# Optimization experiments

Hardware: AMD Instinct MI355X
Metric: run time of the kernel (lower is better)

Reference implementation:

```python
import jax, jax.numpy as jnp
import numpy as np

MODEL_DIM = 768
N_HEAD = 12
HEAD_DIM = MODEL_DIM // N_HEAD
B, S = 2, 2048


def setup_inputs() -> dict:
    key = jax.random.key(0)
    ks = jax.random.split(key, 11)
    sc = 1.0 / np.sqrt(MODEL_DIM)
    inp = {
        "q": jax.random.normal(ks[0], (B, S, MODEL_DIM), jnp.float32),
        "k": jax.random.normal(ks[1], (B, S, MODEL_DIM), jnp.float32),
        "v": jax.random.normal(ks[2], (B, S, MODEL_DIM), jnp.float32),
        "wq_w": jax.random.normal(ks[3], (MODEL_DIM, MODEL_DIM), jnp.float32) * sc,
        "wq_b": jax.random.normal(ks[4], (MODEL_DIM,), jnp.float32) * sc,
        "wk_w": jax.random.normal(ks[5], (MODEL_DIM, MODEL_DIM), jnp.float32) * sc,
        "wk_b": jax.random.normal(ks[6], (MODEL_DIM,), jnp.float32) * sc,
        "wv_w": jax.random.normal(ks[7], (MODEL_DIM, MODEL_DIM), jnp.float32) * sc,
        "wv_b": jax.random.normal(ks[8], (MODEL_DIM,), jnp.float32) * sc,
        "wo_w": jax.random.normal(ks[9], (MODEL_DIM, MODEL_DIM), jnp.float32) * sc,
        "wo_b": jax.random.normal(ks[10], (MODEL_DIM,), jnp.float32) * sc,
    }
    return inp


def _split_heads(x):
    b, s, _ = x.shape
    return x.reshape(b, s, N_HEAD, HEAD_DIM).transpose(0, 2, 1, 3)  # [B,H,S,Dh]


def reference(q, k, v, wq_w, wq_b, wk_w, wk_b, wv_w, wv_b, wo_w, wo_b):
    # Linear projections (torch Linear: x @ W.T + b)
    query = _split_heads(q @ wq_w.T + wq_b)
    key = _split_heads(k @ wk_w.T + wk_b)
    value = _split_heads(v @ wv_w.T + wv_b)
    scale = 1.0 / np.sqrt(HEAD_DIM)
    scores = jnp.einsum("bhqd,bhkd->bhqk", query, key) * scale
    attn_weights = jax.nn.softmax(scores, axis=-1)
    context = jnp.einsum("bhqk,bhkd->bhqd", attn_weights, value)
    b, h, s, dh = context.shape
    context = context.transpose(0, 2, 1, 3).reshape(b, s, MODEL_DIM)
    output = context @ wo_w.T + wo_b
    return output, attn_weights
```

## Files before the change

kernel.cpp:

```cpp
#include <hip/hip_runtime.h>
#include <stdint.h>

#define S_LEN   2048
#define NH      12
#define NBH     24
#define DMODEL  768
#define OUT0    3145728
#define SD      131072
#define WSZ     589824

#define QB_OFF   0
#define KB_OFF   3145728
#define VB_OFF   6291456
#define WQ_OFF   9437184
#define WK_OFF   10027008
#define WV_OFF   10616832
#define WO_OFF   11206656
#define QH_OFF   11796480
#define KH_OFF   14942208
#define VT_OFF   18087936
#define CTX_OFF  21233664

typedef __attribute__((ext_vector_type(4))) float          f32x4;
typedef __attribute__((ext_vector_type(8))) __bf16         bf16x8;
typedef __attribute__((ext_vector_type(4))) float          fl4;
typedef __attribute__((ext_vector_type(4))) unsigned short us4;

__device__ __forceinline__ unsigned short f2bf(float f) {
  union { float f; unsigned u; } x; x.f = f;
  return (unsigned short)((x.u + 0x7FFFu + ((x.u >> 16) & 1u)) >> 16);
}

__device__ __forceinline__ float fexp2(float x) {
#if __has_builtin(__builtin_amdgcn_exp2f)
  return __builtin_amdgcn_exp2f(x);
#else
  return exp2f(x);
#endif
}

__device__ __forceinline__ void gld16(const void* g, void* l) {
  __builtin_amdgcn_global_load_lds((__attribute__((address_space(1))) void*)g,
                                   (__attribute__((address_space(3))) void*)l,
                                   16, 0, 0);
}

#define MFMA(a, b, c) __builtin_amdgcn_mfma_f32_16x16x32_bf16((a), (b), (c), 0, 0, 0)

__global__ __launch_bounds__(256) void cvt_kernel(
    const float* __restrict__ q, const float* __restrict__ k, const float* __restrict__ v,
    const float* __restrict__ wq, const float* __restrict__ wk, const float* __restrict__ wv,
    const float* __restrict__ wo, unsigned short* __restrict__ ws)
{
  const int seg = blockIdx.y;
  const float* src; unsigned short* dst; int n; float sc = 1.0f;
  if      (seg == 0) { src = q;  dst = ws + QB_OFF; n = OUT0; }
  else if (seg == 1) { src = k;  dst = ws + KB_OFF; n = OUT0; }
  else if (seg == 2) { src = v;  dst = ws + VB_OFF; n = OUT0; }
  else if (seg == 3) { src = wq; dst = ws + WQ_OFF; n = WSZ; sc = 0.125f; }
  else if (seg == 4) { src = wk; dst = ws + WK_OFF; n = WSZ; }
  else if (seg == 5) { src = wv; dst = ws + WV_OFF; n = WSZ; }
  else               { src = wo; dst = ws + WO_OFF; n = WSZ; }
  const int i4 = blockIdx.x * blockDim.x + threadIdx.x;
  if (i4 * 4 >= n) return;
  fl4 f = ((const fl4*)src)[i4];
  us4 o;
  o.x = f2bf(f.x * sc); o.y = f2bf(f.y * sc);
  o.z = f2bf(f.z * sc); o.w = f2bf(f.w * sc);
  ((us4*)dst)[i4] = o;
}

__global__ __launch_bounds__(256, 2) void proj_qkv(
    unsigned short* __restrict__ ws, const float* __restrict__ bq,
    const float* __restrict__ bk, const float* __restrict__ bv)
{
  __shared__ __align__(16) unsigned short As[128 * 64];
  __shared__ __align__(16) unsigned short Bs[128 * 64];
  const int mat = blockIdx.z;
  const unsigned short* X = ws + (size_t)mat * OUT0;
  const unsigned short* W = ws + WQ_OFF + (size_t)mat * WSZ;
  const float* bias = (mat == 0) ? bq : ((mat == 1) ? bk : bv);
  const float bsc = (mat == 0) ? 0.125f : 1.0f;
  unsigned short* dst = ws + QH_OFF + (size_t)mat * OUT0;
  const int m0 = blockIdx.y * 128, n0 = blockIdx.x * 128;
  const int tid = threadIdx.x, lane = tid & 63, w = tid >> 6;
  const int wm = w >> 1, wn = w & 1, qd = lane >> 4, ln = lane & 15;
  const int srow = lane >> 3, scol = (lane & 7) * 8;

  f32x4 acc[4][4] = {};
  for (int k0 = 0; k0 < 768; k0 += 64) {
#pragma unroll
    for (int i = 0; i < 4; i++) {
      const int row = (w * 4 + i) * 8 + srow;
      gld16(X + (size_t)(m0 + row) * 768 + k0 + scol, As + (w * 4 + i) * 512);
      gld16(W + (size_t)(n0 + row) * 768 + k0 + scol, Bs + (w * 4 + i) * 512);
    }
    __syncthreads();
    bf16x8 a[4][2], b[4][2];
#pragma unroll
    for (int kst = 0; kst < 2; kst++) {
#pragma unroll
      for (int mt = 0; mt < 4; mt++)
        a[mt][kst] = *(const bf16x8*)(As + (wm * 64 + mt * 16 + ln) * 64 + kst * 32 + qd * 8);
#pragma unroll
      for (int nt = 0; nt < 4; nt++)
        b[nt][kst] = *(const bf16x8*)(Bs + (wn * 64 + nt * 16 + ln) * 64 + kst * 32 + qd * 8);
    }
#pragma unroll
    for (int mt = 0; mt < 4; mt++)
#pragma unroll
      for (int nt = 0; nt < 4; nt++) {
        acc[mt][nt] = MFMA(a[mt][0], b[nt][0], acc[mt][nt]);
        acc[mt][nt] = MFMA(a[mt][1], b[nt][1], acc[mt][nt]);
      }
    __syncthreads();
  }
#pragma unroll
  for (int nt = 0; nt < 4; nt++) {
    const int n = n0 + wn * 64 + nt * 16 + ln;
    const float bvv = bias[n] * bsc;
    const int h = n >> 6, d = n & 63;
    if (mat < 2) {
#pragma unroll
      for (int mt = 0; mt < 4; mt++)
#pragma unroll
        for (int r = 0; r < 4; r++) {
          const int m = m0 + wm * 64 + mt * 16 + qd * 4 + r;
          const int bb = m >> 11, s = m & 2047;
          dst[(size_t)(bb * NH + h) * SD + (size_t)s * 64 + d] = f2bf(acc[mt][nt][r] + bvv);
        }
    } else {
#pragma unroll
      for (int mt = 0; mt < 4; mt++) {
        const int m = m0 + wm * 64 + mt * 16 + qd * 4;
        const int bb = m >> 11, s = m & 2047;
        us4 o;
        o.x = f2bf(acc[mt][nt][0] + bvv); o.y = f2bf(acc[mt][nt][1] + bvv);
        o.z = f2bf(acc[mt][nt][2] + bvv); o.w = f2bf(acc[mt][nt][3] + bvv);
        *(us4*)(dst + (size_t)(bb * NH + h) * SD + (size_t)d * S_LEN + s) = o;
      }
    }
  }
}

__global__ __launch_bounds__(256, 2) void attn_kernel(
    unsigned short* __restrict__ ws, float* __restrict__ attn_out)
{
  __shared__ __align__(16) unsigned short Qs[128 * 64];
  __shared__ __align__(16) unsigned short KP[128 * 136];
  __shared__ __align__(16) unsigned short Vts[64 * 128];
  __shared__ float rsum[128];

  const int bh = blockIdx.y;
  const int i0 = blockIdx.x * 128;
  const unsigned short* Qg = ws + QH_OFF + (size_t)bh * SD + (size_t)i0 * 64;
  const unsigned short* Kg = ws + KH_OFF + (size_t)bh * SD;
  const unsigned short* Vg = ws + VT_OFF + (size_t)bh * SD;
  float* attnB = attn_out + (size_t)bh * S_LEN * S_LEN + (size_t)i0 * S_LEN;
  unsigned short* ctxB = ws + CTX_OFF + ((size_t)(bh / NH) * S_LEN + i0) * DMODEL + (bh % NH) * 64;

  const int tid = threadIdx.x, lane = tid & 63, w = tid >> 6;
  const int wm = w >> 1, wn = w & 1, qd = lane >> 4, ln = lane & 15;
  const float LOG2E = 1.4426950408889634f;

#pragma unroll
  for (int i = 0; i < 4; i++) gld16(Qg + (w * 4 + i) * 512 + lane * 8, Qs + (w * 4 + i) * 512);
  if (tid < 128) rsum[tid] = 0.f;
  __syncthreads();

  bf16x8 aq[4][2];
#pragma unroll
  for (int kst = 0; kst < 2; kst++)
#pragma unroll
    for (int mt = 0; mt < 4; mt++)
      aq[mt][kst] = *(const bf16x8*)(Qs + (wm * 64 + mt * 16 + ln) * 64 + kst * 32 + qd * 8);

  float psum[4][4] = {};
  for (int jt = 0; jt < 16; jt++) {
    const unsigned short* Kt = Kg + jt * 8192;
#pragma unroll
    for (int i = 0; i < 4; i++) gld16(Kt + (w * 4 + i) * 512 + lane * 8, KP + (w * 4 + i) * 512);
    __syncthreads();
    bf16x8 b[4][2];
#pragma unroll
    for (int kst = 0; kst < 2; kst++)
#pragma unroll
      for (int nt = 0; nt < 4; nt++)
        b[nt][kst] = *(const bf16x8*)(KP + (wn * 64 + nt * 16 + ln) * 64 + kst * 32 + qd * 8);
#pragma unroll
    for (int mt = 0; mt < 4; mt++)
#pragma unroll
      for (int nt = 0; nt < 4; nt++) {
        f32x4 c = {0.f, 0.f, 0.f, 0.f};
        c = MFMA(aq[mt][0], b[nt][0], c);
        c = MFMA(aq[mt][1], b[nt][1], c);
#pragma unroll
        for (int r = 0; r < 4; r++) psum[mt][r] += fexp2(c[r] * LOG2E);
      }
    __syncthreads();
  }
#pragma unroll
  for (int mt = 0; mt < 4; mt++)
#pragma unroll
    for (int r = 0; r < 4; r++) {
      float vv = psum[mt][r];
      vv += __shfl_xor(vv, 1); vv += __shfl_xor(vv, 2);
      vv += __shfl_xor(vv, 4); vv += __shfl_xor(vv, 8);
      if (ln == 0) atomicAdd(&rsum[wm * 64 + mt * 16 + qd * 4 + r], vv);
    }
  __syncthreads();
  if (tid < 128) rsum[tid] = 1.0f / rsum[tid];
  __syncthreads();
  float rv[4][4];
#pragma unroll
  for (int mt = 0; mt < 4; mt++)
#pragma unroll
    for (int r = 0; r < 4; r++) rv[mt][r] = rsum[wm * 64 + mt * 16 + qd * 4 + r];

  f32x4 ctx[4][2] = {};
  for (int jt = 0; jt < 16; jt++) {
    const unsigned short* Kt = Kg + jt * 8192;
#pragma unroll
    for (int i = 0; i < 4; i++) {
      gld16(Kt + (w * 4 + i) * 512 + lane * 8, KP + (w * 4 + i) * 512);
      const int d = (w * 4 + i) * 4 + qd;
      gld16(Vg + (size_t)d * S_LEN + jt * 128 + ln * 8, Vts + (w * 4 + i) * 512);
    }
    __syncthreads();
    bf16x8 b[4][2];
#pragma unroll
    for (int kst = 0; kst < 2; kst++)
#pragma unroll
      for (int nt = 0; nt < 4; nt++)
        b[nt][kst] = *(const bf16x8*)(KP + (wn * 64 + nt * 16 + ln) * 64 + kst * 32 + qd * 8);
    float pv[4][4][4];
#pragma unroll
    for (int mt = 0; mt < 4; mt++)
#pragma unroll
      for (int nt = 0; nt < 4; nt++) {
        f32x4 c = {0.f, 0.f, 0.f, 0.f};
        c = MFMA(aq[mt][0], b[nt][0], c);
        c = MFMA(aq[mt][1], b[nt][1], c);
#pragma unroll
        for (int r = 0; r < 4; r++)
          pv[mt][nt][r] = fexp2(c[r] * LOG2E) * rv[mt][r];
      }
#pragma unroll
    for (int mt = 0; mt < 4; mt++)
#pragma unroll
      for (int r = 0; r < 4; r++) {
        float* drow = attnB + (size_t)(wm * 64 + mt * 16 + qd * 4 + r) * S_LEN + jt * 128 + wn * 64 + ln;
#pragma unroll
        for (int nt = 0; nt < 4; nt++) drow[nt * 16] = pv[mt][nt][r];
      }
    __syncthreads();
#pragma unroll
    for (int mt = 0; mt < 4; mt++)
#pragma unroll
      for (int nt = 0; nt < 4; nt++)
#pragma unroll
        for (int r = 0; r < 4; r++)
          KP[(wm * 64 + mt * 16 + qd * 4 + r) * 136 + wn * 64 + nt * 16 + ln] = f2bf(pv[mt][nt][r]);
    __syncthreads();
#pragma unroll
    for (int kst = 0; kst < 4; kst++) {
      bf16x8 pa[4], vb[2];
#pragma unroll
      for (int mt = 0; mt < 4; mt++)
        pa[mt] = *(const bf16x8*)(KP + (wm * 64 + mt * 16 + ln) * 136 + kst * 32 + qd * 8);
#pragma unroll
      for (int nt = 0; nt < 2; nt++)
        vb[nt] = *(const bf16x8*)(Vts + (wn * 32 + nt * 16 + ln) * 128 + kst * 32 + qd * 8);
#pragma unroll
      for (int mt = 0; mt < 4; mt++)
#pragma unroll
        for (int nt = 0; nt < 2; nt++)
          ctx[mt][nt] = MFMA(pa[mt], vb[nt], ctx[mt][nt]);
    }
    __syncthreads();
  }
#pragma unroll
  for (int mt = 0; mt < 4; mt++)
#pragma unroll
    for (int nt = 0; nt < 2; nt++)
#pragma unroll
      for (int r = 0; r < 4; r++) {
        const int row = wm * 64 + mt * 16 + qd * 4 + r;
        ctxB[(size_t)row * DMODEL + wn * 32 + nt * 16 + ln] = f2bf(ctx[mt][nt][r]);
      }
}

__global__ __launch_bounds__(256, 2) void out_proj(
    const unsigned short* __restrict__ ws, const float* __restrict__ wob,
    float* __restrict__ out)
{
  __shared__ __align__(16) unsigned short As[128 * 64];
  __shared__ __align__(16) unsigned short Bs[128 * 64];
  const unsigned short* X = ws + CTX_OFF;
  const unsigned short* W = ws + WO_OFF;
  const int m0 = blockIdx.y * 128, n0 = blockIdx.x * 128;
  const int tid = threadIdx.x, lane = tid & 63, w = tid >> 6;
  const int wm = w >> 1, wn = w & 1, qd = lane >> 4, ln = lane & 15;
  const int srow = lane >> 3, scol = (lane & 7) * 8;

  f32x4 acc[4][4] = {};
  for (int k0 = 0; k0 < 768; k0 += 64) {
#pragma unroll
    for (int i = 0; i < 4; i++) {
      const int row = (w * 4 + i) * 8 + srow;
      gld16(X + (size_t)(m0 + row) * 768 + k0 + scol, As + (w * 4 + i) * 512);
      gld16(W + (size_t)(n0 + row) * 768 + k0 + scol, Bs + (w * 4 + i) * 512);
    }
    __syncthreads();
    bf16x8 a[4][2], b[4][2];
#pragma unroll
    for (int kst = 0; kst < 2; kst++) {
#pragma unroll
      for (int mt = 0; mt < 4; mt++)
        a[mt][kst] = *(const bf16x8*)(As + (wm * 64 + mt * 16 + ln) * 64 + kst * 32 + qd * 8);
#pragma unroll
      for (int nt = 0; nt < 4; nt++)
        b[nt][kst] = *(const bf16x8*)(Bs + (wn * 64 + nt * 16 + ln) * 64 + kst * 32 + qd * 8);
    }
#pragma unroll
    for (int mt = 0; mt < 4; mt++)
#pragma unroll
      for (int nt = 0; nt < 4; nt++) {
        acc[mt][nt] = MFMA(a[mt][0], b[nt][0], acc[mt][nt]);
        acc[mt][nt] = MFMA(a[mt][1], b[nt][1], acc[mt][nt]);
      }
    __syncthreads();
  }
#pragma unroll
  for (int nt = 0; nt < 4; nt++) {
    const int n = n0 + wn * 64 + nt * 16 + ln;
    const float bvv = wob[n];
#pragma unroll
    for (int mt = 0; mt < 4; mt++)
#pragma unroll
      for (int r = 0; r < 4; r++) {
        const int m = m0 + wm * 64 + mt * 16 + qd * 4 + r;
        out[(size_t)m * DMODEL + n] = acc[mt][nt][r] + bvv;
      }
  }
}

extern "C" void kernel_launch(void* const* d_in, const int* in_sizes, int n_in,
                              void* d_out, int out_size, void* d_ws, size_t ws_size,
                              hipStream_t stream)
{
  const float* q  = (const float*)d_in[0];
  const float* k  = (const float*)d_in[1];
  const float* v  = (const float*)d_in[2];
  const float* wq = (const float*)d_in[3];
  const float* bq = (const float*)d_in[4];
  const float* wk = (const float*)d_in[5];
  const float* bk = (const float*)d_in[6];
  const float* wv = (const float*)d_in[7];
  const float* bv = (const float*)d_in[8];
  const float* wo = (const float*)d_in[9];
  const float* bo = (const float*)d_in[10];
  unsigned short* ws = (unsigned short*)d_ws;
  float* out = (float*)d_out;

  cvt_kernel<<<dim3(3072, 7), 256, 0, stream>>>(q, k, v, wq, wk, wv, wo, ws);
  proj_qkv<<<dim3(6, 32, 3), 256, 0, stream>>>(ws, bq, bk, bv);
  attn_kernel<<<dim3(16, 24), 256, 0, stream>>>(ws, out + OUT0);
  out_proj<<<dim3(6, 32), 256, 0, stream>>>(ws, bo, out);
}
```

Baseline: 574.6 us.

## Double-buffer LDS tiles with XOR swizzle and vectorized attn stores in all GEMMs

Adds LDS double buffering with manual vmcnt waits and raw barriers to the projection GEMMs and both attention passes, so the next K/weight tile loads while MFMAs run on the current one. LDS layouts are XOR-swizzled to avoid bank conflicts. The attention kernel swaps the MFMA operand order so each lane holds four consecutive keys, which lets it write attn weights as 16-byte vector stores and reduce row sums with fewer shuffles. It also stages P in a separate swizzled buffer, at the cost of relying on hand-tuned waitcnt values that must match the outstanding load counts.

```diff
diff --git a/kernel.cpp b/kernel.cpp
--- a/kernel.cpp
+++ b/kernel.cpp
@@ -23,6 +23,7 @@
 
 typedef __attribute__((ext_vector_type(4))) float          f32x4;
 typedef __attribute__((ext_vector_type(8))) __bf16         bf16x8;
+typedef __attribute__((ext_vector_type(4))) __bf16         bf16x4;
 typedef __attribute__((ext_vector_type(4))) float          fl4;
 typedef __attribute__((ext_vector_type(4))) unsigned short us4;
 
@@ -46,6 +47,8 @@
 }
 
 #define MFMA(a, b, c) __builtin_amdgcn_mfma_f32_16x16x32_bf16((a), (b), (c), 0, 0, 0)
+#define MEMBAR() asm volatile("" ::: "memory")
+#define SBAR()   __builtin_amdgcn_s_barrier()
 
 __global__ __launch_bounds__(256) void cvt_kernel(
     const float* __restrict__ q, const float* __restrict__ k, const float* __restrict__ v,
@@ -74,8 +77,8 @@
     unsigned short* __restrict__ ws, const float* __restrict__ bq,
     const float* __restrict__ bk, const float* __restrict__ bv)
 {
-  __shared__ __align__(16) unsigned short As[128 * 64];
-  __shared__ __align__(16) unsigned short Bs[128 * 64];
+  __shared__ __align__(16) unsigned short As[2][8192];
+  __shared__ __align__(16) unsigned short Bs[2][8192];
   const int mat = blockIdx.z;
   const unsigned short* X = ws + (size_t)mat * OUT0;
   const unsigned short* W = ws + WQ_OFF + (size_t)mat * WSZ;
@@ -85,26 +88,38 @@
   const int m0 = blockIdx.y * 128, n0 = blockIdx.x * 128;
   const int tid = threadIdx.x, lane = tid & 63, w = tid >> 6;
   const int wm = w >> 1, wn = w & 1, qd = lane >> 4, ln = lane & 15;
-  const int srow = lane >> 3, scol = (lane & 7) * 8;
+  const int srow = lane >> 3, sc8 = ((lane & 7) ^ srow) * 8;
+
+#pragma unroll
+  for (int i = 0; i < 4; i++) {
+    const int row = (w * 4 + i) * 8 + srow;
+    gld16(X + (size_t)(m0 + row) * 768 + sc8, &As[0][(w * 4 + i) * 512]);
+    gld16(W + (size_t)(n0 + row) * 768 + sc8, &Bs[0][(w * 4 + i) * 512]);
+  }
 
   f32x4 acc[4][4] = {};
-  for (int k0 = 0; k0 < 768; k0 += 64) {
+  for (int kk = 0; kk < 12; kk++) {
+    const int knx = (kk == 11) ? 0 : (kk + 1);
+    const int nb = (kk + 1) & 1;
 #pragma unroll
     for (int i = 0; i < 4; i++) {
       const int row = (w * 4 + i) * 8 + srow;
-      gld16(X + (size_t)(m0 + row) * 768 + k0 + scol, As + (w * 4 + i) * 512);
-      gld16(W + (size_t)(n0 + row) * 768 + k0 + scol, Bs + (w * 4 + i) * 512);
-    }
-    __syncthreads();
+      gld16(X + (size_t)(m0 + row) * 768 + knx * 64 + sc8, &As[nb][(w * 4 + i) * 512]);
+      gld16(W + (size_t)(n0 + row) * 768 + knx * 64 + sc8, &Bs[nb][(w * 4 + i) * 512]);
+    }
+    asm volatile("s_waitcnt vmcnt(8)" ::: "memory");
+    SBAR();
+    const unsigned short* Ac = As[kk & 1];
+    const unsigned short* Bc = Bs[kk & 1];
     bf16x8 a[4][2], b[4][2];
 #pragma unroll
     for (int kst = 0; kst < 2; kst++) {
 #pragma unroll
       for (int mt = 0; mt < 4; mt++)
-        a[mt][kst] = *(const bf16x8*)(As + (wm * 64 + mt * 16 + ln) * 64 + kst * 32 + qd * 8);
+        a[mt][kst] = *(const bf16x8*)(Ac + (wm * 64 + mt * 16 + ln) * 64 + (((kst * 4 + qd) ^ (ln & 7)) * 8));
 #pragma unroll
       for (int nt = 0; nt < 4; nt++)
-        b[nt][kst] = *(const bf16x8*)(Bs + (wn * 64 + nt * 16 + ln) * 64 + kst * 32 + qd * 8);
+        b[nt][kst] = *(const bf16x8*)(Bc + (wn * 64 + nt * 16 + ln) * 64 + (((kst * 4 + qd) ^ (ln & 7)) * 8));
     }
 #pragma unroll
     for (int mt = 0; mt < 4; mt++)
@@ -113,7 +128,8 @@
         acc[mt][nt] = MFMA(a[mt][0], b[nt][0], acc[mt][nt]);
         acc[mt][nt] = MFMA(a[mt][1], b[nt][1], acc[mt][nt]);
       }
-    __syncthreads();
+    MEMBAR();
+    SBAR();
   }
 #pragma unroll
   for (int nt = 0; nt < 4; nt++) {
@@ -141,15 +157,19 @@
       }
     }
   }
+  asm volatile("s_waitcnt vmcnt(0)" ::: "memory");
 }
 
 __global__ __launch_bounds__(256, 2) void attn_kernel(
     unsigned short* __restrict__ ws, float* __restrict__ attn_out)
 {
-  __shared__ __align__(16) unsigned short Qs[128 * 64];
-  __shared__ __align__(16) unsigned short KP[128 * 136];
-  __shared__ __align__(16) unsigned short Vts[64 * 128];
-  __shared__ float rsum[128];
+  __shared__ __align__(16) unsigned short lds[40960];
+  unsigned short* K0 = lds;
+  unsigned short* K1 = lds + 8192;
+  unsigned short* Vt = lds + 16384;
+  unsigned short* P  = lds + 24576;
+  float* rsum        = (float*)(lds + 24576);
+  unsigned short* Qs = lds + 32768;
 
   const int bh = blockIdx.y;
   const int i0 = blockIdx.x * 128;
@@ -161,123 +181,149 @@
 
   const int tid = threadIdx.x, lane = tid & 63, w = tid >> 6;
   const int wm = w >> 1, wn = w & 1, qd = lane >> 4, ln = lane & 15;
+  const int srow = lane >> 3, sc8 = ((lane & 7) ^ srow) * 8;
   const float LOG2E = 1.4426950408889634f;
 
 #pragma unroll
-  for (int i = 0; i < 4; i++) gld16(Qg + (w * 4 + i) * 512 + lane * 8, Qs + (w * 4 + i) * 512);
+  for (int i = 0; i < 4; i++) {
+    const int row = (w * 4 + i) * 8 + srow;
+    gld16(Qg + (size_t)row * 64 + sc8, Qs + (w * 4 + i) * 512);
+  }
+  MEMBAR();
+#pragma unroll
+  for (int i = 0; i < 4; i++) {
+    const int row = (w * 4 + i) * 8 + srow;
+    gld16(Kg + (size_t)row * 64 + sc8, K0 + (w * 4 + i) * 512);
+  }
   if (tid < 128) rsum[tid] = 0.f;
-  __syncthreads();
-
-  bf16x8 aq[4][2];
+  asm volatile("s_waitcnt vmcnt(4) lgkmcnt(0)" ::: "memory");
+  SBAR();
+
+  bf16x8 bq[4][2];
 #pragma unroll
   for (int kst = 0; kst < 2; kst++)
 #pragma unroll
-    for (int mt = 0; mt < 4; mt++)
-      aq[mt][kst] = *(const bf16x8*)(Qs + (wm * 64 + mt * 16 + ln) * 64 + kst * 32 + qd * 8);
-
-  float psum[4][4] = {};
+    for (int qt = 0; qt < 4; qt++)
+      bq[qt][kst] = *(const bf16x8*)(Qs + (wm * 64 + qt * 16 + ln) * 64 + (((kst * 4 + qd) ^ (ln & 7)) * 8));
+
+  float psl[4] = {0.f, 0.f, 0.f, 0.f};
   for (int jt = 0; jt < 16; jt++) {
-    const unsigned short* Kt = Kg + jt * 8192;
-#pragma unroll
-    for (int i = 0; i < 4; i++) gld16(Kt + (w * 4 + i) * 512 + lane * 8, KP + (w * 4 + i) * 512);
-    __syncthreads();
-    bf16x8 b[4][2];
+    const unsigned short* Kn = Kg + (size_t)((jt + 1) & 15) * 8192;
+    unsigned short* Kw = (jt & 1) ? K0 : K1;
+#pragma unroll
+    for (int i = 0; i < 4; i++) {
+      const int row = (w * 4 + i) * 8 + srow;
+      gld16(Kn + (size_t)row * 64 + sc8, Kw + (w * 4 + i) * 512);
+    }
+    asm volatile("s_waitcnt vmcnt(4)" ::: "memory");
+    SBAR();
+    const unsigned short* Kc = (jt & 1) ? K1 : K0;
+    bf16x8 ak[4][2];
 #pragma unroll
     for (int kst = 0; kst < 2; kst++)
 #pragma unroll
-      for (int nt = 0; nt < 4; nt++)
-        b[nt][kst] = *(const bf16x8*)(KP + (wn * 64 + nt * 16 + ln) * 64 + kst * 32 + qd * 8);
-#pragma unroll
-    for (int mt = 0; mt < 4; mt++)
-#pragma unroll
-      for (int nt = 0; nt < 4; nt++) {
+      for (int kt = 0; kt < 4; kt++)
+        ak[kt][kst] = *(const bf16x8*)(Kc + (wn * 64 + kt * 16 + ln) * 64 + (((kst * 4 + qd) ^ (ln & 7)) * 8));
+#pragma unroll
+    for (int qt = 0; qt < 4; qt++)
+#pragma unroll
+      for (int kt = 0; kt < 4; kt++) {
         f32x4 c = {0.f, 0.f, 0.f, 0.f};
-        c = MFMA(aq[mt][0], b[nt][0], c);
-        c = MFMA(aq[mt][1], b[nt][1], c);
-#pragma unroll
-        for (int r = 0; r < 4; r++) psum[mt][r] += fexp2(c[r] * LOG2E);
-      }
-    __syncthreads();
-  }
-#pragma unroll
-  for (int mt = 0; mt < 4; mt++)
-#pragma unroll
-    for (int r = 0; r < 4; r++) {
-      float vv = psum[mt][r];
-      vv += __shfl_xor(vv, 1); vv += __shfl_xor(vv, 2);
-      vv += __shfl_xor(vv, 4); vv += __shfl_xor(vv, 8);
-      if (ln == 0) atomicAdd(&rsum[wm * 64 + mt * 16 + qd * 4 + r], vv);
-    }
-  __syncthreads();
-  if (tid < 128) rsum[tid] = 1.0f / rsum[tid];
-  __syncthreads();
-  float rv[4][4];
-#pragma unroll
-  for (int mt = 0; mt < 4; mt++)
-#pragma unroll
-    for (int r = 0; r < 4; r++) rv[mt][r] = rsum[wm * 64 + mt * 16 + qd * 4 + r];
+        c = MFMA(ak[kt][0], bq[qt][0], c);
+        c = MFMA(ak[kt][1], bq[qt][1], c);
+        psl[qt] += fexp2(c[0] * LOG2E) + fexp2(c[1] * LOG2E)
+                 + fexp2(c[2] * LOG2E) + fexp2(c[3] * LOG2E);
+      }
+    MEMBAR();
+    SBAR();
+  }
+#pragma unroll
+  for (int qt = 0; qt < 4; qt++) {
+    float v = psl[qt];
+    v += __shfl_xor(v, 16);
+    v += __shfl_xor(v, 32);
+    psl[qt] = v;
+  }
+  if (lane < 16) {
+#pragma unroll
+    for (int qt = 0; qt < 4; qt++)
+      atomicAdd(&rsum[wm * 64 + qt * 16 + lane], psl[qt]);
+  }
+  asm volatile("s_waitcnt lgkmcnt(0)" ::: "memory");
+  SBAR();
+  float rv[4];
+#pragma unroll
+  for (int qt = 0; qt < 4; qt++) rv[qt] = 1.0f / rsum[wm * 64 + qt * 16 + ln];
 
   f32x4 ctx[4][2] = {};
   for (int jt = 0; jt < 16; jt++) {
-    const unsigned short* Kt = Kg + jt * 8192;
 #pragma unroll
     for (int i = 0; i < 4; i++) {
-      gld16(Kt + (w * 4 + i) * 512 + lane * 8, KP + (w * 4 + i) * 512);
       const int d = (w * 4 + i) * 4 + qd;
-      gld16(Vg + (size_t)d * S_LEN + jt * 128 + ln * 8, Vts + (w * 4 + i) * 512);
-    }
-    __syncthreads();
-    bf16x8 b[4][2];
+      const int csw = ((lane & 15) ^ ((i & 1) * 4 + qd)) * 8;
+      gld16(Vg + (size_t)d * S_LEN + jt * 128 + csw, Vt + (w * 4 + i) * 512);
+    }
+    MEMBAR();
+    const unsigned short* Kn = Kg + (size_t)((jt + 1) & 15) * 8192;
+    unsigned short* Kw = (jt & 1) ? K0 : K1;
+#pragma unroll
+    for (int i = 0; i < 4; i++) {
+      const int row = (w * 4 + i) * 8 + srow;
+      gld16(Kn + (size_t)row * 64 + sc8, Kw + (w * 4 + i) * 512);
+    }
+    asm volatile("s_waitcnt vmcnt(8)" ::: "memory");
+    SBAR();
+
+    const unsigned short* Kc = (jt & 1) ? K1 : K0;
+    bf16x8 ak[4][2];
 #pragma unroll
     for (int kst = 0; kst < 2; kst++)
 #pragma unroll
-      for (int nt = 0; nt < 4; nt++)
-        b[nt][kst] = *(const bf16x8*)(KP + (wn * 64 + nt * 16 + ln) * 64 + kst * 32 + qd * 8);
-    float pv[4][4][4];
-#pragma unroll
-    for (int mt = 0; mt < 4; mt++)
-#pragma unroll
-      for (int nt = 0; nt < 4; nt++) {
+      for (int kt = 0; kt < 4; kt++)
+        ak[kt][kst] = *(const bf16x8*)(Kc + (wn * 64 + kt * 16 + ln) * 64 + (((kst * 4 + qd) ^ (ln & 7)) * 8));
+
+#pragma unroll
+    for (int qt = 0; qt < 4; qt++) {
+      const int qrow = wm * 64 + qt * 16 + ln;
+      float* aRow = attnB + (size_t)qrow * S_LEN + jt * 128 + wn * 64 + qd * 4;
+      unsigned short* pRow = P + qrow * 128;
+      const int r7x8 = (ln & 7) * 8;
+#pragma unroll
+      for (int kt = 0; kt < 4; kt++) {
         f32x4 c = {0.f, 0.f, 0.f, 0.f};
-        c = MFMA(aq[mt][0], b[nt][0], c);
-        c = MFMA(aq[mt][1], b[nt][1], c);
-#pragma unroll
-        for (int r = 0; r < 4; r++)
-          pv[mt][nt][r] = fexp2(c[r] * LOG2E) * rv[mt][r];
-      }
-#pragma unroll
-    for (int mt = 0; mt < 4; mt++)
-#pragma unroll
-      for (int r = 0; r < 4; r++) {
-        float* drow = attnB + (size_t)(wm * 64 + mt * 16 + qd * 4 + r) * S_LEN + jt * 128 + wn * 64 + ln;
-#pragma unroll
-        for (int nt = 0; nt < 4; nt++) drow[nt * 16] = pv[mt][nt][r];
-      }
-    __syncthreads();
-#pragma unroll
-    for (int mt = 0; mt < 4; mt++)
-#pragma unroll
-      for (int nt = 0; nt < 4; nt++)
-#pragma unroll
-        for (int r = 0; r < 4; r++)
-          KP[(wm * 64 + mt * 16 + qd * 4 + r) * 136 + wn * 64 + nt * 16 + ln] = f2bf(pv[mt][nt][r]);
-    __syncthreads();
+        c = MFMA(ak[kt][0], bq[qt][0], c);
+        c = MFMA(ak[kt][1], bq[qt][1], c);
+        f32x4 pv;
+        pv.x = fexp2(c[0] * LOG2E) * rv[qt];
+        pv.y = fexp2(c[1] * LOG2E) * rv[qt];
+        pv.z = fexp2(c[2] * LOG2E) * rv[qt];
+        pv.w = fexp2(c[3] * LOG2E) * rv[qt];
+        *(f32x4*)(aRow + kt * 16) = pv;
+        bf16x4 pb;
+        pb.x = (__bf16)pv.x; pb.y = (__bf16)pv.y;
+        pb.z = (__bf16)pv.z; pb.w = (__bf16)pv.w;
+        *(bf16x4*)(pRow + ((wn * 64 + kt * 16 + qd * 4) ^ r7x8)) = pb;
+      }
+    }
+    asm volatile("s_waitcnt vmcnt(20) lgkmcnt(0)" ::: "memory");
+    SBAR();
 #pragma unroll
     for (int kst = 0; kst < 4; kst++) {
       bf16x8 pa[4], vb[2];
 #pragma unroll
       for (int mt = 0; mt < 4; mt++)
-        pa[mt] = *(const bf16x8*)(KP + (wm * 64 + mt * 16 + ln) * 136 + kst * 32 + qd * 8);
+        pa[mt] = *(const bf16x8*)(P + (wm * 64 + mt * 16 + ln) * 128 + ((kst * 32 + qd * 8) ^ ((ln & 7) * 8)));
 #pragma unroll
       for (int nt = 0; nt < 2; nt++)
-        vb[nt] = *(const bf16x8*)(Vts + (wn * 32 + nt * 16 + ln) * 128 + kst * 32 + qd * 8);
+        vb[nt] = *(const bf16x8*)(Vt + (wn * 32 + nt * 16 + ln) * 128 + (((kst * 4 + qd) ^ (ln & 7)) * 8));
 #pragma unroll
       for (int mt = 0; mt < 4; mt++)
 #pragma unroll
         for (int nt = 0; nt < 2; nt++)
           ctx[mt][nt] = MFMA(pa[mt], vb[nt], ctx[mt][nt]);
     }
-    __syncthreads();
+    MEMBAR();
+    SBAR();
   }
 #pragma unroll
   for (int mt = 0; mt < 4; mt++)
@@ -288,39 +334,52 @@
         const int row = wm * 64 + mt * 16 + qd * 4 + r;
         ctxB[(size_t)row * DMODEL + wn * 32 + nt * 16 + ln] = f2bf(ctx[mt][nt][r]);
       }
+  asm volatile("s_waitcnt vmcnt(0)" ::: "memory");
 }
 
 __global__ __launch_bounds__(256, 2) void out_proj(
     const unsigned short* __restrict__ ws, const float* __restrict__ wob,
     float* __restrict__ out)
 {
-  __shared__ __align__(16) unsigned short As[128 * 64];
-  __shared__ __align__(16) unsigned short Bs[128 * 64];
+  __shared__ __align__(16) unsigned short As[2][8192];
+  __shared__ __align__(16) unsigned short Bs[2][8192];
   const unsigned short* X = ws + CTX_OFF;
   const unsigned short* W = ws + WO_OFF;
   const int m0 = blockIdx.y * 128, n0 = blockIdx.x * 128;
   const int tid = threadIdx.x, lane = tid & 63, w = tid >> 6;
   const int wm = w >> 1, wn = w & 1, qd = lane >> 4, ln = lane & 15;
-  const int srow = lane >> 3, scol = (lane & 7) * 8;
+  const int srow = lane >> 3, sc8 = ((lane & 7) ^ srow) * 8;
+
+#pragma unroll
+  for (int i = 0; i < 4; i++) {
+    const int row = (w * 4 + i) * 8 + srow;
+    gld16(X + (size_t)(m0 + row) * 768 + sc8, &As[0][(w * 4 + i) * 512]);
+    gld16(W + (size_t)(n0 + row) * 768 + sc8, &Bs[0][(w * 4 + i) * 512]);
+  }
 
   f32x4 acc[4][4] = {};
-  for (int k0 = 0; k0 < 768; k0 += 64) {
+  for (int kk = 0; kk < 12; kk++) {
+    const int knx = (kk == 11) ? 0 : (kk + 1);
+    const int nb = (kk + 1) & 1;
 #pragma unroll
     for (int i = 0; i < 4; i++) {
       const int row = (w * 4 + i) * 8 + srow;
-      gld16(X + (size_t)(m0 + row) * 768 + k0 + scol, As + (w * 4 + i) * 512);
-      gld16(W + (size_t)(n0 + row) * 768 + k0 + scol, Bs + (w * 4 + i) * 512);
-    }
-    __syncthreads();
+      gld16(X + (size_t)(m0 + row) * 768 + knx * 64 + sc8, &As[nb][(w * 4 + i) * 512]);
+      gld16(W + (size_t)(n0 + row) * 768 + knx * 64 + sc8, &Bs[nb][(w * 4 + i) * 512]);
+    }
+    asm volatile("s_waitcnt vmcnt(8)" ::: "memory");
+    SBAR();
+    const unsigned short* Ac = As[kk & 1];
+    const unsigned short* Bc = Bs[kk & 1];
     bf16x8 a[4][2], b[4][2];
 #pragma unroll
     for (int kst = 0; kst < 2; kst++) {
 #pragma unroll
       for (int mt = 0; mt < 4; mt++)
-        a[mt][kst] = *(const bf16x8*)(As + (wm * 64 + mt * 16 + ln) * 64 + kst * 32 + qd * 8);
+        a[mt][kst] = *(const bf16x8*)(Ac + (wm * 64 + mt * 16 + ln) * 64 + (((kst * 4 + qd) ^ (ln & 7)) * 8));
 #pragma unroll
       for (int nt = 0; nt < 4; nt++)
-        b[nt][kst] = *(const bf16x8*)(Bs + (wn * 64 + nt * 16 + ln) * 64 + kst * 32 + qd * 8);
+        b[nt][kst] = *(const bf16x8*)(Bc + (wn * 64 + nt * 16 + ln) * 64 + (((kst * 4 + qd) ^ (ln & 7)) * 8));
     }
 #pragma unroll
     for (int mt = 0; mt < 4; mt++)
@@ -329,7 +388,8 @@
         acc[mt][nt] = MFMA(a[mt][0], b[nt][0], acc[mt][nt]);
         acc[mt][nt] = MFMA(a[mt][1], b[nt][1], acc[mt][nt]);
       }
-    __syncthreads();
+    MEMBAR();
+    SBAR();
   }
 #pragma unroll
   for (int nt = 0; nt < 4; nt++) {
@@ -343,6 +403,7 @@
         out[(size_t)m * DMODEL + n] = acc[mt][nt][r] + bvv;
       }
   }
+  asm volatile("s_waitcnt vmcnt(0)" ::: "memory");
 }
 
 extern "C" void kernel_launch(void* const* d_in, const int* in_sizes, int n_in,
```

New measurement: 569.0 us. Within noise of the previous version (-1.0%).
